# Optimization experiments

Hardware: AMD Instinct MI355X
Metric: run time of the kernel (lower is better)

## Reference

```python
import jax, jax.numpy as jnp
import numpy as np

# Each of the 16 binary logic gates, relaxed to real values, is a multilinear
# function: gate(a,b) = c0 + c1*a + c2*b + c3*a*b. Rows follow the standard
# difflogic ordering: FALSE, AND, a&~b, a, ~a&b, b, XOR, OR, NOR, XNOR,
# ~b, a|~b, ~a, ~a|b, NAND, TRUE.
GATE_COEF = jnp.array([
    [0.0,  0.0,  0.0,  0.0],   # 0:  false
    [0.0,  0.0,  0.0,  1.0],   # 1:  a AND b
    [0.0,  1.0,  0.0, -1.0],   # 2:  a AND NOT b
    [0.0,  1.0,  0.0,  0.0],   # 3:  a
    [0.0,  0.0,  1.0, -1.0],   # 4:  NOT a AND b
    [0.0,  0.0,  1.0,  0.0],   # 5:  b
    [0.0,  1.0,  1.0, -2.0],   # 6:  a XOR b
    [0.0,  1.0,  1.0, -1.0],   # 7:  a OR b
    [1.0, -1.0, -1.0,  1.0],   # 8:  NOR
    [1.0, -1.0, -1.0,  2.0],   # 9:  XNOR
    [1.0,  0.0, -1.0,  0.0],   # 10: NOT b
    [1.0,  0.0, -1.0,  1.0],   # 11: a OR NOT b
    [1.0, -1.0,  0.0,  0.0],   # 12: NOT a
    [1.0, -1.0,  0.0,  1.0],   # 13: NOT a OR b
    [1.0,  0.0,  0.0, -1.0],   # 14: NAND
    [1.0,  0.0,  0.0,  0.0],   # 15: true
], dtype=jnp.float32)

B, IN_DIM, HIDDEN, N_LAYERS, OUT_DIM, TAU = 4096, 1024, 8192, 6, 8, 10.0
NPO = HIDDEN // OUT_DIM  # neurons_per_output


def logic_layer(h, w, ia, ib):
    # h: [B, in_dim]; w: [H, 16]; ia, ib: [H] int indices into in_dim.
    # Softmax-weighted blend of 16 gates == multilinear form with blended coefs.
    p = jax.nn.softmax(w, axis=-1)          # [H, 16]
    c = p @ GATE_COEF                       # [H, 4]
    a = h[:, ia]                            # [B, H] gather
    b = h[:, ib]                            # [B, H] gather
    return c[:, 0] + c[:, 1] * a + c[:, 2] * b + c[:, 3] * (a * b)


def setup_inputs() -> dict:
    key = jax.random.key(0)
    ks = jax.random.split(key, 8)
    return {
        "x": jax.random.uniform(ks[0], (B, IN_DIM), dtype=jnp.float32),
        "logic_w": jax.random.normal(ks[1], (N_LAYERS, HIDDEN, 16), dtype=jnp.float32),
        "scaler_w": jax.random.normal(ks[2], (OUT_DIM, OUT_DIM), dtype=jnp.float32) * 0.1,
        "scaler_b": jax.random.normal(ks[3], (OUT_DIM,), dtype=jnp.float32) * 0.1,
        "idx0_a": jax.random.randint(ks[4], (HIDDEN,), 0, IN_DIM, dtype=jnp.int32),
        "idx0_b": jax.random.randint(ks[5], (HIDDEN,), 0, IN_DIM, dtype=jnp.int32),
        "idx_a": jax.random.randint(ks[6], (N_LAYERS - 1, HIDDEN), 0, HIDDEN, dtype=jnp.int32),
        "idx_b": jax.random.randint(ks[7], (N_LAYERS - 1, HIDDEN), 0, HIDDEN, dtype=jnp.int32),
    }


def reference(x, logic_w, scaler_w, scaler_b, idx0_a, idx0_b, idx_a, idx_b):
    h = (x.reshape(x.shape[0], -1) > 0.5).astype(jnp.float32)   # binarize
    h = logic_layer(h, logic_w[0], idx0_a, idx0_b)               # [B, HIDDEN]
    for i in range(N_LAYERS - 1):
        h = logic_layer(h, logic_w[i + 1], idx_a[i], idx_b[i])
    h = h.reshape(h.shape[0], OUT_DIM, NPO)                      # [B, O, NPO]
    values = jnp.sum(h, axis=2) / TAU                            # [B, O]
    q_values = values @ scaler_w.T + scaler_b                    # nn.Linear
    return q_values
```

## Files before the change

### kernel.cpp

```cpp
#include <hip/hip_runtime.h>
#include <hip/hip_fp16.h>

constexpr int BATCH    = 4096;
constexpr int IN_DIM   = 1024;
constexpr int HIDDEN   = 8192;
constexpr int N_LAYERS = 6;
constexpr int OUT_DIM  = 8;
constexpr float INV_TAU = 0.1f;

constexpr int TB   = 8;
constexpr int NTH  = 1024;
constexpr int NPT  = HIDDEN / NTH;
constexpr int NWAVES = NTH / 64;

__device__ __forceinline__ __half2 u2h(unsigned int u) {
    union { unsigned int u; __half2 h; } v; v.u = u; return v.h;
}
__device__ __forceinline__ unsigned int h2u(__half2 h) {
    union { unsigned int u; __half2 h; } v; v.h = h; return v.u;
}

__device__ __forceinline__ uint2 pack4(float4 v) {
    __half2 lo = __float22half2_rn(make_float2(v.x, v.y));
    __half2 hi = __float22half2_rn(make_float2(v.z, v.w));
    uint2 r; r.x = h2u(lo); r.y = h2u(hi); return r;
}

__global__ void prep_kernel(const float* __restrict__ logic_w,
                            const int* __restrict__ idx0_a,
                            const int* __restrict__ idx0_b,
                            const int* __restrict__ idx_a,
                            const int* __restrict__ idx_b,
                            uint2* __restrict__ coefp,
                            unsigned int* __restrict__ idxp, int n)
{
    int id = blockIdx.x * blockDim.x + threadIdx.x;
    if (id >= n) return;
    const int l = id / HIDDEN;
    const int j = id - l * HIDDEN;

    int ia, ib;
    if (l == 0) { ia = idx0_a[j]; ib = idx0_b[j]; }
    else        { ia = idx_a[(size_t)(l - 1) * HIDDEN + j];
                  ib = idx_b[(size_t)(l - 1) * HIDDEN + j]; }
    idxp[id] = (unsigned int)ia | ((unsigned int)ib << 16);

    const float4* w4 = (const float4*)(logic_w + (size_t)id * 16);
    float4 wa = w4[0], wb = w4[1], wc = w4[2], wd = w4[3];
    float wv[16] = {wa.x, wa.y, wa.z, wa.w, wb.x, wb.y, wb.z, wb.w,
                    wc.x, wc.y, wc.z, wc.w, wd.x, wd.y, wd.z, wd.w};
    float m = wv[0];
#pragma unroll
    for (int i = 1; i < 16; ++i) m = fmaxf(m, wv[i]);
    float e[16];
    float s = 0.f;
#pragma unroll
    for (int i = 0; i < 16; ++i) { e[i] = expf(wv[i] - m); s += e[i]; }
    float inv = 1.f / s;
    const float G0[16] = {0,0,0,0,0,0,0,0, 1,1,1,1,1,1,1,1};
    const float G1[16] = {0,0,1,1,0,0,1,1, -1,-1,0,0,-1,-1,0,0};
    const float G2[16] = {0,0,0,0,1,1,1,1, -1,-1,-1,-1,0,0,0,0};
    const float G3[16] = {0,1,-1,0,-1,0,-2,-1, 1,2,0,1,0,1,-1,0};
    float c0 = 0.f, c1 = 0.f, c2 = 0.f, c3 = 0.f;
#pragma unroll
    for (int i = 0; i < 16; ++i) {
        float p = e[i] * inv;
        c0 = fmaf(p, G0[i], c0);
        c1 = fmaf(p, G1[i], c1);
        c2 = fmaf(p, G2[i], c2);
        c3 = fmaf(p, G3[i], c3);
    }
    coefp[id] = pack4(make_float4(c0, c1, c2, c3));
}

__device__ __forceinline__ uint4 gate8(uint4 a, uint4 b, uint2 c) {
    __half2 cp01 = u2h(c.x), cp23 = u2h(c.y);
    __half2 c0 = __low2half2(cp01), c1 = __high2half2(cp01);
    __half2 c2 = __low2half2(cp23), c3 = __high2half2(cp23);
    uint4 r;
    {
        __half2 av = u2h(a.x), bv = u2h(b.x);
        r.x = h2u(__hfma2(bv, __hfma2(c3, av, c2), __hfma2(c1, av, c0)));
    }
    {
        __half2 av = u2h(a.y), bv = u2h(b.y);
        r.y = h2u(__hfma2(bv, __hfma2(c3, av, c2), __hfma2(c1, av, c0)));
    }
    {
        __half2 av = u2h(a.z), bv = u2h(b.z);
        r.z = h2u(__hfma2(bv, __hfma2(c3, av, c2), __hfma2(c1, av, c0)));
    }
    {
        __half2 av = u2h(a.w), bv = u2h(b.w);
        r.w = h2u(__hfma2(bv, __hfma2(c3, av, c2), __hfma2(c1, av, c0)));
    }
    return r;
}

__global__ __launch_bounds__(NTH) void net_kernel(
    const float*  __restrict__ x,
    const uint2*  __restrict__ coefp,
    const unsigned int* __restrict__ idxp,
    const float*  __restrict__ scaler_w, const float* __restrict__ scaler_b,
    float* __restrict__ out)
{
    __shared__ uint4 h[HIDDEN];
    __shared__ uint4 hx[IN_DIM];
    __shared__ float warr[NWAVES][TB];
    __shared__ float vals[TB][OUT_DIM];

    const int tid = threadIdx.x;
    const int b0  = blockIdx.x * TB;

    {
        float v[TB];
#pragma unroll
        for (int r = 0; r < TB; ++r)
            v[r] = (x[(size_t)(b0 + r) * IN_DIM + tid] > 0.5f) ? 1.f : 0.f;
        uint4 p;
        p.x = h2u(__floats2half2_rn(v[0], v[1]));
        p.y = h2u(__floats2half2_rn(v[2], v[3]));
        p.z = h2u(__floats2half2_rn(v[4], v[5]));
        p.w = h2u(__floats2half2_rn(v[6], v[7]));
        hx[tid] = p;
    }

    uint4 acc[NPT];
    unsigned int ij[NPT], ijn[NPT];
    uint2 cf[NPT], cfn[NPT];

#pragma unroll
    for (int k = 0; k < NPT; ++k) { ij[k] = idxp[k * NTH + tid]; cf[k] = coefp[k * NTH + tid]; }

    __syncthreads();

#pragma unroll
    for (int k = 0; k < NPT; ++k) {
        ijn[k] = idxp[HIDDEN + k * NTH + tid];
        cfn[k] = coefp[HIDDEN + k * NTH + tid];
    }
#pragma unroll
    for (int k = 0; k < NPT; ++k) {
        unsigned int pr = ij[k];
        acc[k] = gate8(hx[pr & 0xffffu], hx[pr >> 16], cf[k]);
    }
#pragma unroll
    for (int k = 0; k < NPT; ++k) h[k * NTH + tid] = acc[k];
    __syncthreads();

    for (int l = 1; l < N_LAYERS; ++l) {
#pragma unroll
        for (int k = 0; k < NPT; ++k) { ij[k] = ijn[k]; cf[k] = cfn[k]; }
        if (l < N_LAYERS - 1) {
#pragma unroll
            for (int k = 0; k < NPT; ++k) {
                ijn[k] = idxp[(size_t)(l + 1) * HIDDEN + k * NTH + tid];
                cfn[k] = coefp[(size_t)(l + 1) * HIDDEN + k * NTH + tid];
            }
        }
#pragma unroll
        for (int k = 0; k < NPT; ++k) {
            unsigned int pr = ij[k];
            acc[k] = gate8(h[pr & 0xffffu], h[pr >> 16], cf[k]);
        }
        __syncthreads();
#pragma unroll
        for (int k = 0; k < NPT; ++k) h[k * NTH + tid] = acc[k];
        __syncthreads();
    }

    {
        const int k    = tid >> 7;
        const int base = k * 1024 + (tid & 127);
        float s[TB] = {0.f, 0.f, 0.f, 0.f, 0.f, 0.f, 0.f, 0.f};
#pragma unroll
        for (int i = 0; i < 8; ++i) {
            uint4 t = h[base + 128 * i];
            float2 f0 = __half22float2(u2h(t.x));
            float2 f1 = __half22float2(u2h(t.y));
            float2 f2 = __half22float2(u2h(t.z));
            float2 f3 = __half22float2(u2h(t.w));
            s[0] += f0.x; s[1] += f0.y; s[2] += f1.x; s[3] += f1.y;
            s[4] += f2.x; s[5] += f2.y; s[6] += f3.x; s[7] += f3.y;
        }
#pragma unroll
        for (int off = 32; off > 0; off >>= 1) {
#pragma unroll
            for (int r = 0; r < TB; ++r) s[r] += __shfl_down(s[r], off);
        }
        if ((tid & 63) == 0) {
#pragma unroll
            for (int r = 0; r < TB; ++r) warr[tid >> 6][r] = s[r];
        }
    }
    __syncthreads();
    if (tid < TB * OUT_DIM) {
        int r = tid >> 3;
        int k = tid & 7;
        vals[r][k] = (warr[2 * k][r] + warr[2 * k + 1][r]) * INV_TAU;
    }
    __syncthreads();
    if (tid < TB * OUT_DIM) {
        int r = tid >> 3;
        int o = tid & 7;
        float q = scaler_b[o];
#pragma unroll
        for (int k = 0; k < OUT_DIM; ++k)
            q = fmaf(vals[r][k], scaler_w[o * OUT_DIM + k], q);
        out[(size_t)(b0 + r) * OUT_DIM + o] = q;
    }
}

extern "C" void kernel_launch(void* const* d_in, const int* in_sizes, int n_in,
                              void* d_out, int out_size, void* d_ws, size_t ws_size,
                              hipStream_t stream)
{
    const float* x        = (const float*)d_in[0];
    const float* logic_w  = (const float*)d_in[1];
    const float* scaler_w = (const float*)d_in[2];
    const float* scaler_b = (const float*)d_in[3];
    const int*   idx0_a   = (const int*)d_in[4];
    const int*   idx0_b   = (const int*)d_in[5];
    const int*   idx_a    = (const int*)d_in[6];
    const int*   idx_b    = (const int*)d_in[7];
    float* out = (float*)d_out;

    const int n = N_LAYERS * HIDDEN;
    uint2*        coefp = (uint2*)d_ws;
    unsigned int* idxp  = (unsigned int*)((char*)d_ws + (size_t)n * sizeof(uint2));

    prep_kernel<<<(n + 255) / 256, 256, 0, stream>>>(logic_w, idx0_a, idx0_b,
                                                     idx_a, idx_b, coefp, idxp, n);
    net_kernel<<<BATCH / TB, NTH, 0, stream>>>(x, coefp, idxp,
                                               scaler_w, scaler_b, out);
}
```

Measured before the change: 117.7 us.

## Fuse pairs of logic layers by composing gate indices and coefficients in prep

Each pair of consecutive logic layers is collapsed into one stage. The prep kernel composes the bottom layer's indices through the top layer's indices, giving four source indices per output neuron, and precomputes the coefficients of both feeding gates plus the top gate. The net kernel then evaluates three gates per neuron directly from the stage input. This halves the number of shared-memory write/sync rounds and stage loops, at the cost of recomputing the bottom-layer gates redundantly (three gate evaluations per neuron per stage instead of two), doing four gathers instead of four across two stages, and loading more coefficient data per stage.

```diff
diff --git a/kernel.cpp b/kernel.cpp
--- a/kernel.cpp
+++ b/kernel.cpp
@@ -5,6 +5,7 @@
 constexpr int IN_DIM   = 1024;
 constexpr int HIDDEN   = 8192;
 constexpr int N_LAYERS = 6;
+constexpr int N_STAGES = N_LAYERS / 2;
 constexpr int OUT_DIM  = 8;
 constexpr float INV_TAU = 0.1f;
 
@@ -26,26 +27,9 @@
     uint2 r; r.x = h2u(lo); r.y = h2u(hi); return r;
 }
 
-__global__ void prep_kernel(const float* __restrict__ logic_w,
-                            const int* __restrict__ idx0_a,
-                            const int* __restrict__ idx0_b,
-                            const int* __restrict__ idx_a,
-                            const int* __restrict__ idx_b,
-                            uint2* __restrict__ coefp,
-                            unsigned int* __restrict__ idxp, int n)
-{
-    int id = blockIdx.x * blockDim.x + threadIdx.x;
-    if (id >= n) return;
-    const int l = id / HIDDEN;
-    const int j = id - l * HIDDEN;
-
-    int ia, ib;
-    if (l == 0) { ia = idx0_a[j]; ib = idx0_b[j]; }
-    else        { ia = idx_a[(size_t)(l - 1) * HIDDEN + j];
-                  ib = idx_b[(size_t)(l - 1) * HIDDEN + j]; }
-    idxp[id] = (unsigned int)ia | ((unsigned int)ib << 16);
-
-    const float4* w4 = (const float4*)(logic_w + (size_t)id * 16);
+__device__ __forceinline__ uint2 softmax_coef(const float* __restrict__ logic_w,
+                                              int l, int p) {
+    const float4* w4 = (const float4*)(logic_w + ((size_t)l * HIDDEN + p) * 16);
     float4 wa = w4[0], wb = w4[1], wc = w4[2], wd = w4[3];
     float wv[16] = {wa.x, wa.y, wa.z, wa.w, wb.x, wb.y, wb.z, wb.w,
                     wc.x, wc.y, wc.z, wc.w, wd.x, wd.y, wd.z, wd.w};
@@ -64,13 +48,52 @@
     float c0 = 0.f, c1 = 0.f, c2 = 0.f, c3 = 0.f;
 #pragma unroll
     for (int i = 0; i < 16; ++i) {
-        float p = e[i] * inv;
-        c0 = fmaf(p, G0[i], c0);
-        c1 = fmaf(p, G1[i], c1);
-        c2 = fmaf(p, G2[i], c2);
-        c3 = fmaf(p, G3[i], c3);
-    }
-    coefp[id] = pack4(make_float4(c0, c1, c2, c3));
+        float pv = e[i] * inv;
+        c0 = fmaf(pv, G0[i], c0);
+        c1 = fmaf(pv, G1[i], c1);
+        c2 = fmaf(pv, G2[i], c2);
+        c3 = fmaf(pv, G3[i], c3);
+    }
+    return pack4(make_float4(c0, c1, c2, c3));
+}
+
+__global__ void prep_kernel(const float* __restrict__ logic_w,
+                            const int* __restrict__ idx0_a,
+                            const int* __restrict__ idx0_b,
+                            const int* __restrict__ idx_a,
+                            const int* __restrict__ idx_b,
+                            uint4* __restrict__ cABp,
+                            uint2* __restrict__ idx4p,
+                            uint2* __restrict__ cCp, int n)
+{
+    int id = blockIdx.x * blockDim.x + threadIdx.x;
+    if (id >= n) return;
+    const int s = id >> 13;
+    const int j = id & (HIDDEN - 1);
+    const int ltop = 2 * s + 1;
+    const int lbot = 2 * s;
+
+    const int pa = idx_a[(size_t)(ltop - 1) * HIDDEN + j];
+    const int pb = idx_b[(size_t)(ltop - 1) * HIDDEN + j];
+
+    int gaa, gba, gab, gbb;
+    if (s == 0) {
+        gaa = idx0_a[pa]; gba = idx0_b[pa];
+        gab = idx0_a[pb]; gbb = idx0_b[pb];
+    } else {
+        const int* A  = idx_a + (size_t)(lbot - 1) * HIDDEN;
+        const int* Bv = idx_b + (size_t)(lbot - 1) * HIDDEN;
+        gaa = A[pa]; gba = Bv[pa];
+        gab = A[pb]; gbb = Bv[pb];
+    }
+    idx4p[id] = make_uint2((unsigned)gaa | ((unsigned)gba << 16),
+                           (unsigned)gab | ((unsigned)gbb << 16));
+
+    uint2 cA = softmax_coef(logic_w, lbot, pa);
+    uint2 cB = softmax_coef(logic_w, lbot, pb);
+    uint2 cC = softmax_coef(logic_w, ltop, j);
+    cABp[id] = make_uint4(cA.x, cA.y, cB.x, cB.y);
+    cCp[id]  = cC;
 }
 
 __device__ __forceinline__ uint4 gate8(uint4 a, uint4 b, uint2 c) {
@@ -99,8 +122,9 @@
 
 __global__ __launch_bounds__(NTH) void net_kernel(
     const float*  __restrict__ x,
-    const uint2*  __restrict__ coefp,
-    const unsigned int* __restrict__ idxp,
+    const uint4*  __restrict__ cABp,
+    const uint2*  __restrict__ idx4p,
+    const uint2*  __restrict__ cCp,
     const float*  __restrict__ scaler_w, const float* __restrict__ scaler_b,
     float* __restrict__ out)
 {
@@ -125,43 +149,50 @@
         hx[tid] = p;
     }
 
+    uint2 ij[NPT], ijn[NPT];
     uint4 acc[NPT];
-    unsigned int ij[NPT], ijn[NPT];
-    uint2 cf[NPT], cfn[NPT];
-
-#pragma unroll
-    for (int k = 0; k < NPT; ++k) { ij[k] = idxp[k * NTH + tid]; cf[k] = coefp[k * NTH + tid]; }
-
-    __syncthreads();
-
+
+#pragma unroll
+    for (int k = 0; k < NPT; ++k) ij[k] = idx4p[k * NTH + tid];
+
+    __syncthreads();
+
+#pragma unroll
+    for (int k = 0; k < NPT; ++k) ijn[k] = idx4p[HIDDEN + k * NTH + tid];
 #pragma unroll
     for (int k = 0; k < NPT; ++k) {
-        ijn[k] = idxp[HIDDEN + k * NTH + tid];
-        cfn[k] = coefp[HIDDEN + k * NTH + tid];
-    }
-#pragma unroll
-    for (int k = 0; k < NPT; ++k) {
-        unsigned int pr = ij[k];
-        acc[k] = gate8(hx[pr & 0xffffu], hx[pr >> 16], cf[k]);
+        uint2 p = ij[k];
+        uint4 x1 = hx[p.x & 0xffffu], x2 = hx[p.x >> 16];
+        uint4 x3 = hx[p.y & 0xffffu], x4 = hx[p.y >> 16];
+        uint4 cab = cABp[k * NTH + tid];
+        uint2 cc  = cCp[k * NTH + tid];
+        uint4 u = gate8(x1, x2, make_uint2(cab.x, cab.y));
+        uint4 v = gate8(x3, x4, make_uint2(cab.z, cab.w));
+        acc[k] = gate8(u, v, cc);
     }
 #pragma unroll
     for (int k = 0; k < NPT; ++k) h[k * NTH + tid] = acc[k];
     __syncthreads();
 
-    for (int l = 1; l < N_LAYERS; ++l) {
-#pragma unroll
-        for (int k = 0; k < NPT; ++k) { ij[k] = ijn[k]; cf[k] = cfn[k]; }
-        if (l < N_LAYERS - 1) {
-#pragma unroll
-            for (int k = 0; k < NPT; ++k) {
-                ijn[k] = idxp[(size_t)(l + 1) * HIDDEN + k * NTH + tid];
-                cfn[k] = coefp[(size_t)(l + 1) * HIDDEN + k * NTH + tid];
-            }
+#pragma unroll
+    for (int s = 1; s < N_STAGES; ++s) {
+#pragma unroll
+        for (int k = 0; k < NPT; ++k) ij[k] = ijn[k];
+        if (s < N_STAGES - 1) {
+#pragma unroll
+            for (int k = 0; k < NPT; ++k)
+                ijn[k] = idx4p[(size_t)(s + 1) * HIDDEN + k * NTH + tid];
         }
 #pragma unroll
         for (int k = 0; k < NPT; ++k) {
-            unsigned int pr = ij[k];
-            acc[k] = gate8(h[pr & 0xffffu], h[pr >> 16], cf[k]);
+            uint2 p = ij[k];
+            uint4 x1 = h[p.x & 0xffffu], x2 = h[p.x >> 16];
+            uint4 x3 = h[p.y & 0xffffu], x4 = h[p.y >> 16];
+            uint4 cab = cABp[(size_t)s * HIDDEN + k * NTH + tid];
+            uint2 cc  = cCp[(size_t)s * HIDDEN + k * NTH + tid];
+            uint4 u = gate8(x1, x2, make_uint2(cab.x, cab.y));
+            uint4 v = gate8(x3, x4, make_uint2(cab.z, cab.w));
+            acc[k] = gate8(u, v, cc);
         }
         __syncthreads();
 #pragma unroll
@@ -225,12 +256,13 @@
     const int*   idx_b    = (const int*)d_in[7];
     float* out = (float*)d_out;
 
-    const int n = N_LAYERS * HIDDEN;
-    uint2*        coefp = (uint2*)d_ws;
-    unsigned int* idxp  = (unsigned int*)((char*)d_ws + (size_t)n * sizeof(uint2));
-
-    prep_kernel<<<(n + 255) / 256, 256, 0, stream>>>(logic_w, idx0_a, idx0_b,
-                                                     idx_a, idx_b, coefp, idxp, n);
-    net_kernel<<<BATCH / TB, NTH, 0, stream>>>(x, coefp, idxp,
+    const int n = N_STAGES * HIDDEN;
+    uint4* cABp = (uint4*)d_ws;
+    uint2* idx4p = (uint2*)((char*)d_ws + (size_t)n * sizeof(uint4));
+    uint2* cCp   = (uint2*)((char*)d_ws + (size_t)n * (sizeof(uint4) + sizeof(uint2)));
+
+    prep_kernel<<<(n + 127) / 128, 128, 0, stream>>>(logic_w, idx0_a, idx0_b,
+                                                     idx_a, idx_b, cABp, idx4p, cCp, n);
+    net_kernel<<<BATCH / TB, NTH, 0, stream>>>(x, cABp, idx4p, cCp,
                                                scaler_w, scaler_b, out);
 }
```

Measured after the change: 115.8 us. About the same (-1.6%).
